# Kernel tuning notes

Hardware: AMD Instinct MI355X
Metric: run time of the kernel (lower is better)

The kernel has to match this reference:

```python
import jax, jax.numpy as jnp
import numpy as np

B, S, D = 2, 1024, 768
H, HD = 12, 64
E, K, F = 8, 2, 3072
EPS = 1e-5


def _ln(x, g, b):
    mu = jnp.mean(x, -1, keepdims=True)
    var = jnp.mean(jnp.square(x - mu), -1, keepdims=True)
    return (x - mu) * jax.lax.rsqrt(var + EPS) * g + b


def setup_inputs() -> dict:
    key = jax.random.key(0)
    ks = jax.random.split(key, 12)
    s = lambda k, shape, sc: jax.random.normal(k, shape, jnp.float32) * sc
    return {
        "hidden_states": s(ks[0], (B, S, D), 1.0),
        "ln1_g": jnp.ones((D,), jnp.float32), "ln1_b": jnp.zeros((D,), jnp.float32),
        "w_attn": s(ks[1], (D, 3 * D), 0.02), "b_attn": jnp.zeros((3 * D,), jnp.float32),
        "w_attnproj": s(ks[2], (D, D), 0.02), "b_attnproj": jnp.zeros((D,), jnp.float32),
        "ln2_g": jnp.ones((D,), jnp.float32), "ln2_b": jnp.zeros((D,), jnp.float32),
        "w_router": s(ks[3], (E, D), 0.01),
        "w_fc": s(ks[4], (E, D, F), 0.02 / E), "b_fc": jnp.zeros((E, F), jnp.float32),
        "w_proj": s(ks[5], (E, F, D), 0.02 / E), "b_proj": jnp.zeros((E, D), jnp.float32),
    }


def reference(hidden_states, ln1_g, ln1_b, w_attn, b_attn, w_attnproj, b_attnproj,
              ln2_g, ln2_b, w_router, w_fc, b_fc, w_proj, b_proj):
    # --- attention sub-block (GPT-2 style, causal) ---
    residual = hidden_states
    x = _ln(hidden_states, ln1_g, ln1_b)
    qkv = x @ w_attn + b_attn                         # [B,S,3D]
    q, k, v = jnp.split(qkv, 3, axis=-1)
    def heads(t):
        return t.reshape(B, S, H, HD).transpose(0, 2, 1, 3)  # [B,H,S,HD]
    q, k, v = heads(q), heads(k), heads(v)
    scores = jnp.einsum("bhqd,bhkd->bhqk", q, k) / np.sqrt(HD).astype(np.float32)
    causal = jnp.tril(jnp.ones((S, S), bool))
    scores = jnp.where(causal, scores, jnp.finfo(scores.dtype).min)
    attn = jax.nn.softmax(scores, axis=-1)
    ctx = jnp.einsum("bhqk,bhkd->bhqd", attn, v)
    ctx = ctx.transpose(0, 2, 1, 3).reshape(B, S, D)
    attn_out = ctx @ w_attnproj + b_attnproj
    hs = attn_out + residual

    # --- MoE FFN sub-block ---
    residual = hs
    x2 = _ln(hs, ln2_g, ln2_b)
    logits = x2 @ w_router.T                          # [B,S,E]
    probs = jax.nn.softmax(logits, axis=-1)
    top_w, top_idx = jax.lax.top_k(probs, K)          # [B,S,K]
    top_w = top_w / jnp.sum(top_w, -1, keepdims=True)
    gates = jnp.sum(jax.nn.one_hot(top_idx, E, dtype=x2.dtype) * top_w[..., None], axis=2)  # [B,S,E]
    h = jax.nn.gelu(jnp.einsum("bsd,edf->bsef", x2, w_fc) + b_fc, approximate=False)
    y = jnp.einsum("bsef,efd->bsed", h, w_proj) + b_proj
    moe_out = jnp.einsum("bse,bsed->bsd", gates, y)
    return moe_out + residual
```

## Files before the change

kernel.cpp:

```cpp
#include <hip/hip_runtime.h>
#include <hip/hip_bf16.h>
#include <math.h>

#define NB 2
#define SEQ 1024
#define DM 768
#define NHEAD 12
#define HDIM 64
#define NEXP 8
#define FF 3072
#define NTOK (NB*SEQ)
#define TDIM (3*DM)
#define LNEPS 1e-5f
#define NSLOT (NTOK*2)

typedef __attribute__((ext_vector_type(8))) short v8s;
typedef __attribute__((ext_vector_type(4))) float v4f;

#define GLDS16(src, dst) \
    __builtin_amdgcn_global_load_lds((const __attribute__((address_space(1))) unsigned int*)(src), \
                                     (__attribute__((address_space(3))) unsigned int*)(dst), 16, 0, 0)

static __device__ __forceinline__ float bf2f(unsigned short u){
    return __uint_as_float(((unsigned)u) << 16);
}
static __device__ __forceinline__ unsigned short f2bf(float f){
    unsigned u = __float_as_uint(f);
    u += 0x7fffu + ((u >> 16) & 1u);
    return (unsigned short)(u >> 16);
}
static __device__ __forceinline__ float gelu_exact(float x){
    return 0.5f * x * (1.0f + erff(x * 0.70710678118654752440f));
}

__global__ __launch_bounds__(256) void tconv_kernel(const float* __restrict__ in,
                                                    unsigned short* __restrict__ out,
                                                    int R, int C){
    __shared__ float T[32][33];
    size_t base = (size_t)blockIdx.z * R * C;
    int c0 = blockIdx.x * 32, r0 = blockIdx.y * 32;
    int t = threadIdx.x;
    int tr = t >> 3, tc4 = (t & 7) * 4;
    float4 v = *(const float4*)&in[base + (size_t)(r0 + tr) * C + c0 + tc4];
    T[tr][tc4+0] = v.x; T[tr][tc4+1] = v.y; T[tr][tc4+2] = v.z; T[tr][tc4+3] = v.w;
    __syncthreads();
    int oc = t >> 3, or4 = (t & 7) * 4;
    ushort4 o;
    o.x = f2bf(T[or4+0][oc]); o.y = f2bf(T[or4+1][oc]);
    o.z = f2bf(T[or4+2][oc]); o.w = f2bf(T[or4+3][oc]);
    *(ushort4*)&out[base + (size_t)(c0 + oc) * R + r0 + or4] = o;
}

__global__ __launch_bounds__(256) void ln_b(const float* __restrict__ in,
                                            const float* __restrict__ g,
// ... 80 lines not shown
    }
    __syncthreads();
    if (tid == 0){
        float lg[NEXP];
        #pragma unroll
        for (int e = 0; e < NEXP; e++)
            lg[e] = wsum[0][e] + wsum[1][e] + wsum[2][e] + wsum[3][e];
        int i0 = 0; float m0 = lg[0];
        #pragma unroll
        for (int e = 1; e < NEXP; e++) if (lg[e] > m0){ m0 = lg[e]; i0 = e; }
        int i1 = -1; float m1 = -INFINITY;
        #pragma unroll
        for (int e = 0; e < NEXP; e++) if (e != i0 && lg[e] > m1){ m1 = lg[e]; i1 = e; }
        float mx = fmaxf(m0, m1);
        float e0 = __expf(m0 - mx), e1 = __expf(m1 - mx);
        float inv = 1.0f / (e0 + e1);
        int p0 = atomicAdd(&cnt[i0], 1);
        int p1 = atomicAdd(&cnt[i1], 1);
        expTok[i0*NTOK + p0] = t;
        expTok[i1*NTOK + p1] = t;
        tokE[t*2]   = i0; tokE[t*2+1]   = i1;
        tokPos[t*2] = p0; tokPos[t*2+1] = p1;
        tokGate[t*2]   = e0 * inv;
        tokGate[t*2+1] = e1 * inv;
    }
}

__global__ __launch_bounds__(256) void mm_qkv(const unsigned short* __restrict__ Ab,
                                              const unsigned short* __restrict__ Bb,
                                              const float* __restrict__ bias,
                                              unsigned short* __restrict__ Qb,
                                              unsigned short* __restrict__ Kb,
                                              unsigned short* __restrict__ Vt){
    __shared__ __align__(16) unsigned short As[64*32];
    __shared__ __align__(16) unsigned short Bs[128*32];
    int bm = blockIdx.y * 64, bn = blockIdx.x * 128;
    int tid = threadIdx.x, wave = tid >> 6, lane = tid & 63;
    int quad = lane >> 4, l15 = lane & 15;
    int wm = wave >> 1, wn = wave & 1;
    int arow = tid >> 2, achunk = (tid & 3) * 8;
    int lrow = lane >> 2, lchunk = (lane & 3) * 8;
    const unsigned short* aS  = Ab + (size_t)(bm + arow) * DM + achunk;
    const unsigned short* bS0 = Bb + (size_t)(bn +      wave*16 + lrow) * DM + lchunk;
    const unsigned short* bS1 = Bb + (size_t)(bn + 64 + wave*16 + lrow) * DM + lchunk;
    unsigned short* aD  = &As[(wave*16)*32];
    unsigned short* bD0 = &Bs[(     wave*16)*32];
    unsigned short* bD1 = &Bs[(64 + wave*16)*32];
    v4f acc[2][4];
    #pragma unroll
    for (int i = 0; i < 2; i++)
        #pragma unroll
        for (int j = 0; j < 4; j++) acc[i][j] = (v4f){0.f,0.f,0.f,0.f};
    for (int kt = 0; kt < DM/32; kt++){
        int kb = kt * 32;
        GLDS16(aS + kb, aD); GLDS16(bS0 + kb, bD0); GLDS16(bS1 + kb, bD1);
        __syncthreads();
        v8s a[2], bfr[4];
        #pragma unroll
        for (int i = 0; i < 2; i++) a[i] = *(const v8s*)&As[(wm*32 + i*16 + l15)*32 + quad*8];
        #pragma unroll
        for (int i = 0; i < 4; i++) bfr[i] = *(const v8s*)&Bs[(wn*64 + i*16 + l15)*32 + quad*8];
        #pragma unroll
        for (int mi = 0; mi < 2; mi++)
            #pragma unroll
            for (int ni = 0; ni < 4; ni++)
                acc[mi][ni] = __builtin_amdgcn_mfma_f32_16x16x32_bf16(a[mi], bfr[ni], acc[mi][ni], 0, 0, 0);
        __syncthreads();
    }
    int btyp = bn / DM;
    #pragma unroll
    for (int ni = 0; ni < 4; ni++){
        int n = bn + wn*64 + ni*16 + l15;
        float bb = bias[n];
        int hd = n % DM; int h = hd >> 6; int d = hd & 63;
        #pragma unroll
        for (int mi = 0; mi < 2; mi++){
            int m = bm + wm*32 + mi*16 + quad*4;
            int b = m >> 10, sd = m & 1023;
            size_t bhbase = (size_t)(b*NHEAD + h);
            if (btyp == 0){
                #pragma unroll
                for (int r = 0; r < 4; r++)
                    Qb[(bhbase*SEQ + sd + r)*HDIM + d] = f2bf((acc[mi][ni][r] + bb) * 0.125f);
            } else if (btyp == 1){
                #pragma unroll
                for (int r = 0; r < 4; r++)
                    Kb[(bhbase*SEQ + sd + r)*HDIM + d] = f2bf(acc[mi][ni][r] + bb);
            } else {
                ushort4 o;
                o.x = f2bf(acc[mi][ni][0] + bb); o.y = f2bf(acc[mi][ni][1] + bb);
                o.z = f2bf(acc[mi][ni][2] + bb); o.w = f2bf(acc[mi][ni][3] + bb);
                *(ushort4*)&Vt[(bhbase*HDIM + d)*SEQ + sd] = o;
            }
        }
    }
}

__global__ __launch_bounds__(64) void fattn(const unsigned short* __restrict__ Qb,
                                            const unsigned short* __restrict__ Kb,
                                            const unsigned short* __restrict__ Vt,
                                            unsigned short* __restrict__ ctxb){
    int bh = blockIdx.x >> 5;
    int q0 = (31 - (blockIdx.x & 31)) * 32;
    int h = bh % NHEAD, b = bh / NHEAD;
    int lane = threadIdx.x;
    int quad = lane >> 4, l15 = lane & 15;

    __shared__ __align__(16) unsigned short Plds[32*32];

    const unsigned short* qp = Qb + ((size_t)bh*SEQ + q0 + l15) * HDIM + quad*8;
    v8s qa00 = *(const v8s*)qp;
    v8s qa01 = *(const v8s*)(qp + 32);
    v8s qa10 = *(const v8s*)(qp + 16*HDIM);
    v8s qa11 = *(const v8s*)(qp + 16*HDIM + 32);

    v4f o[2][4];
    #pragma unroll
    for (int i = 0; i < 2; i++)
        #pragma unroll
        for (int j = 0; j < 4; j++) o[i][j] = (v4f){0.f,0.f,0.f,0.f};
    float mrow[2][4], lrow[2][4];
    #pragma unroll
    for (int i = 0; i < 2; i++)
        #pragma unroll
        for (int r = 0; r < 4; r++){ mrow[i][r] = -1e30f; lrow[i][r] = 0.f; }

    int nch = (q0 >> 5) + 1;
    for (int ch = 0; ch < nch; ch++){
        int kt = ch * 32;
        const unsigned short* kp = Kb + ((size_t)bh*SEQ + kt + l15) * HDIM + quad*8;
        v8s k00 = *(const v8s*)kp;
        v8s k01 = *(const v8s*)(kp + 32);
        v8s k10 = *(const v8s*)(kp + 16*HDIM);
        v8s k11 = *(const v8s*)(kp + 16*HDIM + 32);
        v4f s00 = {0,0,0,0}, s01 = {0,0,0,0}, s10 = {0,0,0,0}, s11 = {0,0,0,0};
        s00 = __builtin_amdgcn_mfma_f32_16x16x32_bf16(qa00, k00, s00, 0, 0, 0);
        s00 = __builtin_amdgcn_mfma_f32_16x16x32_bf16(qa01, k01, s00, 0, 0, 0);
        s01 = __builtin_amdgcn_mfma_f32_16x16x32_bf16(qa00, k10, s01, 0, 0, 0);
        s01 = __builtin_amdgcn_mfma_f32_16x16x32_bf16(qa01, k11, s01, 0, 0, 0);
        s10 = __builtin_amdgcn_mfma_f32_16x16x32_bf16(qa10, k00, s10, 0, 0, 0);
        s10 = __builtin_amdgcn_mfma_f32_16x16x32_bf16(qa11, k01, s10, 0, 0, 0);
        s11 = __builtin_amdgcn_mfma_f32_16x16x32_bf16(qa10, k10, s11, 0, 0, 0);
        s11 = __builtin_amdgcn_mfma_f32_16x16x32_bf16(qa11, k11, s11, 0, 0, 0);

        int key0 = kt + l15, key1 = kt + 16 + l15;
        float alpha[2][4];
        #pragma unroll
        for (int mi = 0; mi < 2; mi++){
            #pragma unroll
            for (int r = 0; r < 4; r++){
                int qrow = q0 + mi*16 + quad*4 + r;
                float sv0 = mi ? s10[r] : s00[r];
                float sv1 = mi ? s11[r] : s01[r];
                float v0 = (key0 <= qrow) ? sv0 : -1e30f;
                float v1 = (key1 <= qrow) ? sv1 : -1e30f;
                float mx = fmaxf(v0, v1);
                mx = fmaxf(mx, __shfl_xor(mx, 1));
                mx = fmaxf(mx, __shfl_xor(mx, 2));
                mx = fmaxf(mx, __shfl_xor(mx, 4));
                mx = fmaxf(mx, __shfl_xor(mx, 8));
                float mn = fmaxf(mrow[mi][r], mx);
                alpha[mi][r] = __expf(mrow[mi][r] - mn);
                float p0 = __expf(v0 - mn);
                float p1 = __expf(v1 - mn);
                float ps = p0 + p1;
                ps += __shfl_xor(ps, 1);
                ps += __shfl_xor(ps, 2);
                ps += __shfl_xor(ps, 4);
                ps += __shfl_xor(ps, 8);
                lrow[mi][r] = lrow[mi][r] * alpha[mi][r] + ps;
                mrow[mi][r] = mn;
                Plds[(mi*16 + quad*4 + r)*32 + l15]      = f2bf(p0);
                Plds[(mi*16 + quad*4 + r)*32 + 16 + l15] = f2bf(p1);
            }
        }
        #pragma unroll
        for (int mi = 0; mi < 2; mi++)
            #pragma unroll
            for (int df = 0; df < 4; df++)
                #pragma unroll
                for (int r = 0; r < 4; r++)
                    o[mi][df][r] *= alpha[mi][r];
        __syncthreads();
        v8s pa0 = *(const v8s*)&Plds[l15*32 + quad*8];
        v8s pa1 = *(const v8s*)&Plds[(16 + l15)*32 + quad*8];
        const unsigned short* vp = Vt + ((size_t)bh*HDIM + l15) * SEQ + kt + quad*8;
        #pragma unroll
        for (int df = 0; df < 4; df++){
            v8s vb = *(const v8s*)(vp + df*16*SEQ);
            o[0][df] = __builtin_amdgcn_mfma_f32_16x16x32_bf16(pa0, vb, o[0][df], 0, 0, 0);
            o[1][df] = __builtin_amdgcn_mfma_f32_16x16x32_bf16(pa1, vb, o[1][df], 0, 0, 0);
        }
        __syncthreads();
    }
    #pragma unroll
    for (int mi = 0; mi < 2; mi++){
        #pragma unroll
        for (int r = 0; r < 4; r++){
            float inv = 1.0f / lrow[mi][r];
            size_t orow = (size_t)(b*SEQ + q0 + mi*16 + quad*4 + r) * DM + h*HDIM;
            #pragma unroll
            for (int df = 0; df < 4; df++)
                ctxb[orow + df*16 + l15] = f2bf(o[mi][df][r] * inv);
        }
    }
}

__global__ __launch_bounds__(256) void mm_attnproj(const unsigned short* __restrict__ Ab,
                                                   const unsigned short* __restrict__ Bb,
                                                   const float* __restrict__ bias,
                                                   const float* __restrict__ res,
                                                   float* __restrict__ C){
    __shared__ __align__(16) unsigned short As[64*32];
    __shared__ __align__(16) unsigned short Bs[64*32];
    int bm = blockIdx.y * 64, bn = blockIdx.x * 64;
    int tid = threadIdx.x, wave = tid >> 6, lane = tid & 63;
    int quad = lane >> 4, l15 = lane & 15;
    int wm = wave >> 1, wn = wave & 1;
    int arow = tid >> 2, achunk = (tid & 3) * 8;
    const unsigned short* aS = Ab + (size_t)(bm + arow) * DM + achunk;
    const unsigned short* bS = Bb + (size_t)(bn + arow) * DM + achunk;
    unsigned short* aD = &As[(wave*16)*32];
    unsigned short* bD = &Bs[(wave*16)*32];
    v4f acc[2][2];
    #pragma unroll
    for (int i = 0; i < 2; i++)
        #pragma unroll
        for (int j = 0; j < 2; j++) acc[i][j] = (v4f){0.f,0.f,0.f,0.f};
    for (int kt = 0; kt < DM/32; kt++){
        int kb = kt * 32;
        GLDS16(aS + kb, aD); GLDS16(bS + kb, bD);
        __syncthreads();
        v8s a[2], bfr[2];
        #pragma unroll
        for (int i = 0; i < 2; i++){
            a[i]   = *(const v8s*)&As[(wm*32 + i*16 + l15)*32 + quad*8];
            bfr[i] = *(const v8s*)&Bs[(wn*32 + i*16 + l15)*32 + quad*8];
        }
        #pragma unroll
        for (int mi = 0; mi < 2; mi++)
            #pragma unroll
            for (int ni = 0; ni < 2; ni++)
                acc[mi][ni] = __builtin_amdgcn_mfma_f32_16x16x32_bf16(a[mi], bfr[ni], acc[mi][ni], 0, 0, 0);
        __syncthreads();
    }
    #pragma unroll
    for (int ni = 0; ni < 2; ni++){
        int n = bn + wn*32 + ni*16 + l15;
        float bb = bias[n];
        #pragma unroll
        for (int mi = 0; mi < 2; mi++){
            int m = bm + wm*32 + mi*16 + quad*4;
            #pragma unroll
            for (int r = 0; r < 4; r++)
                C[(size_t)(m + r) * DM + n] = acc[mi][ni][r] + bb + res[(size_t)(m + r) * DM + n];
        }
    }
}

__global__ __launch_bounds__(256) void mm_fc(const unsigned short* __restrict__ Xb,
                                             const unsigned short* __restrict__ Wb,
                                             const float* __restrict__ bfc,
                                             const int* __restrict__ expTok,
                                             const int* __restrict__ cnt,
                                             const int* __restrict__ offE,
                                             unsigned short* __restrict__ H){
    int e = blockIdx.z, tile = blockIdx.y;
    int c = cnt[e];
    int rows = c - tile * 128;
    if (rows <= 0) return;
    __shared__ __align__(16) unsigned short As[128*32];
    __shared__ __align__(16) unsigned short Bs[128*32];
    __shared__ int toks[128];
    int bn = blockIdx.x * 128;
    int tid = threadIdx.x, wave = tid >> 6, lane = tid & 63;
    if (tid < 128){
        int idx = tile * 128 + tid;
        if (idx >= c) idx = c - 1;
        toks[tid] = expTok[e * NTOK + idx];
    }
    __syncthreads();
    int quad = lane >> 4, l15 = lane & 15;
    int wm = wave >> 1, wn = wave & 1;
    int lrow = lane >> 2, lchunk = (lane & 3) * 8;
    int tok0 = toks[     wave*16 + lrow];
    int tok1 = toks[64 + wave*16 + lrow];
    const unsigned short* Be = Wb + (size_t)e * FF * DM;
    const unsigned short* aS0 = Xb + (size_t)tok0 * DM + lchunk;
    const unsigned short* aS1 = Xb + (size_t)tok1 * DM + lchunk;
    const unsigned short* bS0 = Be + (size_t)(bn +      wave*16 + lrow) * DM + lchunk;
    const unsigned short* bS1 = Be + (size_t)(bn + 64 + wave*16 + lrow) * DM + lchunk;
    unsigned short* aD0 = &As[(     wave*16)*32];
    unsigned short* aD1 = &As[(64 + wave*16)*32];
    unsigned short* bD0 = &Bs[(     wave*16)*32];
    unsigned short* bD1 = &Bs[(64 + wave*16)*32];
    v4f acc[4][4];
    #pragma unroll
    for (int i = 0; i < 4; i++)
        #pragma unroll
        for (int j = 0; j < 4; j++) acc[i][j] = (v4f){0.f,0.f,0.f,0.f};
    for (int kt = 0; kt < DM/32; kt++){
        int kb = kt * 32;
        GLDS16(aS0 + kb, aD0); GLDS16(aS1 + kb, aD1);
        GLDS16(bS0 + kb, bD0); GLDS16(bS1 + kb, bD1);
        __syncthreads();
        v8s a[4], bfr[4];
        #pragma unroll
        for (int i = 0; i < 4; i++){
            a[i]   = *(const v8s*)&As[(wm*64 + i*16 + l15)*32 + quad*8];
            bfr[i] = *(const v8s*)&Bs[(wn*64 + i*16 + l15)*32 + quad*8];
        }
        #pragma unroll
        for (int mt = 0; mt < 4; mt++)
            #pragma unroll
            for (int nt = 0; nt < 4; nt++)
                acc[mt][nt] = __builtin_amdgcn_mfma_f32_16x16x32_bf16(a[mt], bfr[nt], acc[mt][nt], 0, 0, 0);
        __syncthreads();
    }
    int slot0 = offE[e] + tile * 128;
    #pragma unroll
    for (int nt = 0; nt < 4; nt++){
        int n = bn + wn*64 + nt*16 + l15;
        float bb = bfc[(size_t)e * FF + n];
        #pragma unroll
        for (int mt = 0; mt < 4; mt++){
            int ml = wm*64 + mt*16 + quad*4;
            #pragma unroll
            for (int r = 0; r < 4; r++)
                if (ml + r < rows)
                    H[(size_t)(slot0 + ml + r) * FF + n] = f2bf(gelu_exact(acc[mt][nt][r] + bb));
        }
    }
}

__global__ __launch_bounds__(256) void mm_proj(const unsigned short* __restrict__ H,
                                               const unsigned short* __restrict__ Wb,
                                               const int* __restrict__ cnt,
                                               const int* __restrict__ offE,
                                               float* __restrict__ Yp){
    int e = blockIdx.z, tile = blockIdx.y;
    int c = cnt[e];
    int rows = c - tile * 64;
    if (rows <= 0) return;
    int sk = blockIdx.x & 1;
    int bn = (blockIdx.x >> 1) * 128;
    __shared__ __align__(16) unsigned short As[64*32];
    __shared__ __align__(16) unsigned short Bs[128*32];
    int tid = threadIdx.x, wave = tid >> 6, lane = tid & 63;
    int quad = lane >> 4, l15 = lane & 15;
    int wm = wave >> 1, wn = wave & 1;
    int slot0 = offE[e] + tile * 64;
    int arow = tid >> 2, achunk = (tid & 3) * 8;
    int arl = arow < rows ? arow : rows - 1;
    int lrow = lane >> 2, lchunk = (lane & 3) * 8;
    const unsigned short* Be = Wb + (size_t)e * DM * FF;
    const unsigned short* aS  = H  + (size_t)(slot0 + arl) * FF + sk*1536 + achunk;
    const unsigned short* bS0 = Be + (size_t)(bn +      wave*16 + lrow) * FF + sk*1536 + lchunk;
    const unsigned short* bS1 = Be + (size_t)(bn + 64 + wave*16 + lrow) * FF + sk*1536 + lchunk;
    unsigned short* aD  = &As[(wave*16)*32];
    unsigned short* bD0 = &Bs[(     wave*16)*32];
    unsigned short* bD1 = &Bs[(64 + wave*16)*32];
    v4f acc[2][4];
    #pragma unroll
    for (int i = 0; i < 2; i++)
        #pragma unroll
        for (int j = 0; j < 4; j++) acc[i][j] = (v4f){0.f,0.f,0.f,0.f};
    for (int kt = 0; kt < 1536/32; kt++){
        int kb = kt * 32;
        GLDS16(aS + kb, aD); GLDS16(bS0 + kb, bD0); GLDS16(bS1 + kb, bD1);
        __syncthreads();
        v8s a[2], bfr[4];
        #pragma unroll
        for (int i = 0; i < 2; i++) a[i] = *(const v8s*)&As[(wm*32 + i*16 + l15)*32 + quad*8];
        #pragma unroll
        for (int i = 0; i < 4; i++) bfr[i] = *(const v8s*)&Bs[(wn*64 + i*16 + l15)*32 + quad*8];
        #pragma unroll
        for (int mi = 0; mi < 2; mi++)
            #pragma unroll
            for (int ni = 0; ni < 4; ni++)
                acc[mi][ni] = __builtin_amdgcn_mfma_f32_16x16x32_bf16(a[mi], bfr[ni], acc[mi][ni], 0, 0, 0);
        __syncthreads();
    }
    float* Yo = Yp + (size_t)sk * NSLOT * DM;
    #pragma unroll
    for (int ni = 0; ni < 4; ni++){
        int n = bn + wn*64 + ni*16 + l15;
        #pragma unroll
        for (int mi = 0; mi < 2; mi++){
            int ml = wm*32 + mi*16 + quad*4;
            #pragma unroll
            for (int r = 0; r < 4; r++)
                if (ml + r < rows)
                    Yo[(size_t)(slot0 + ml + r) * DM + n] = acc[mi][ni][r];
        }
    }
}

__global__ void offsets_kernel(const int* __restrict__ cnt, int* __restrict__ offE){
    if (threadIdx.x == 0 && blockIdx.x == 0){
        int a = 0;
        for (int e = 0; e < NEXP; e++){ offE[e] = a; a += cnt[e]; }
    }
}

__global__ __launch_bounds__(256) void combine_kernel(const float* __restrict__ hs,
                                                      const float* __restrict__ Yp,
                                                      const float* __restrict__ bproj,
                                                      const int* __restrict__ tokE,
                                                      const int* __restrict__ tokPos,
                                                      const float* __restrict__ tokGate,
                                                      const int* __restrict__ offE,
                                                      float* __restrict__ out){
    int t = blockIdx.x;
    int e0 = tokE[t*2], e1 = tokE[t*2+1];
// ... 33 lines not shown
    const float* b_proj  = (const float*)d_in[13];
    float* out = (float*)d_out;

    char* ws = (char*)d_ws;
    float*          hs   = (float*)(ws + 0);
    unsigned short* xb   = (unsigned short*)(ws + 6291456);
    unsigned short* Qb   = (unsigned short*)(ws + 9437184);
    unsigned short* Kb   = (unsigned short*)(ws + 12582912);
    unsigned short* Vt   = (unsigned short*)(ws + 15728640);
    unsigned short* ctxb = (unsigned short*)(ws + 18874368);
    unsigned short* Wab  = (unsigned short*)(ws + 22020096);
    unsigned short* Wapb = (unsigned short*)(ws + 25559040);
    unsigned short* H    = (unsigned short*)(ws + 9437184);
    unsigned short* Wfcb = (unsigned short*)(ws + 34603008);
    unsigned short* Wprb = (unsigned short*)(ws + 72351744);
    float*          Yp   = (float*)(ws + 34603008);
    char* rt = ws + 110100480;
    int* cnt      = (int*)(rt + 0);
    int* offE     = (int*)(rt + 64);
    int* expTok   = (int*)(rt + 128);
    int* tokE     = (int*)(rt + 128 + 65536);
    int* tokPos   = (int*)(rt + 128 + 81920);
    float* tokGate= (float*)(rt + 128 + 98304);

    hipMemsetAsync(cnt, 0, NEXP * sizeof(int), stream);

    tconv_kernel<<<dim3(TDIM/32, DM/32, 1), 256, 0, stream>>>(w_attn, Wab, DM, TDIM);
    tconv_kernel<<<dim3(DM/32, DM/32, 1), 256, 0, stream>>>(w_aproj, Wapb, DM, DM);
    tconv_kernel<<<dim3(FF/32, DM/32, NEXP), 256, 0, stream>>>(w_fc, Wfcb, DM, FF);
    tconv_kernel<<<dim3(DM/32, FF/32, NEXP), 256, 0, stream>>>(w_proj, Wprb, FF, DM);

    ln_b<<<NTOK, 256, 0, stream>>>(hidden, ln1_g, ln1_b, xb);
    mm_qkv<<<dim3(TDIM/128, NTOK/64), 256, 0, stream>>>(xb, Wab, b_attn, Qb, Kb, Vt);
    fattn<<<NB*NHEAD*32, 64, 0, stream>>>(Qb, Kb, Vt, ctxb);
    mm_attnproj<<<dim3(DM/64, NTOK/64), 256, 0, stream>>>(ctxb, Wapb, b_aproj, hidden, hs);
    ln_router<<<NTOK, 256, 0, stream>>>(hs, ln2_g, ln2_b, w_rout, xb,
                                        cnt, expTok, tokE, tokPos, tokGate);
    offsets_kernel<<<1, 64, 0, stream>>>(cnt, offE);
    mm_fc<<<dim3(FF/128, NTOK/128, NEXP), 256, 0, stream>>>(xb, Wfcb, b_fc, expTok, cnt, offE, H);
    mm_proj<<<dim3((DM/128)*2, NTOK/64, NEXP), 256, 0, stream>>>(H, Wprb, cnt, offE, Yp);
    combine_kernel<<<NTOK, 256, 0, stream>>>(hs, Yp, b_proj, tokE, tokPos, tokGate, offE, out);
}
```

Baseline: 483.6 us.

## Double-buffer LDS tiles with async global-to-LDS prefetch in all GEMM kernels

Converts the QKV, attention-projection, expert FC and expert projection GEMM loops from single-buffered LDS staging to a two-stage ping-pong scheme. The next K-slice is issued with global_load_lds while the current one is being consumed by MFMAs, using explicit vmcnt waits and raw barriers. The goal is to hide global memory latency behind matrix math. In exchange, LDS use per block doubles, which may lower occupancy, and the hand-written waitcnt counts must match the number of outstanding loads for the results to stay correct.

```diff
diff --git a/kernel.cpp b/kernel.cpp
--- a/kernel.cpp
+++ b/kernel.cpp
@@ -20,6 +20,9 @@
 #define GLDS16(src, dst) \
     __builtin_amdgcn_global_load_lds((const __attribute__((address_space(1))) unsigned int*)(src), \
                                      (__attribute__((address_space(3))) unsigned int*)(dst), 16, 0, 0)
+
+#define BARF() do { asm volatile("" ::: "memory"); __builtin_amdgcn_s_barrier(); asm volatile("" ::: "memory"); } while(0)
+#define WAITV(n) asm volatile("s_waitcnt vmcnt(" #n ")" ::: "memory")
 
 static __device__ __forceinline__ float bf2f(unsigned short u){
     return __uint_as_float(((unsigned)u) << 16);
@@ -166,8 +169,8 @@
                                               unsigned short* __restrict__ Qb,
                                               unsigned short* __restrict__ Kb,
                                               unsigned short* __restrict__ Vt){
-    __shared__ __align__(16) unsigned short As[64*32];
-    __shared__ __align__(16) unsigned short Bs[128*32];
+    __shared__ __align__(16) unsigned short As[2][64*32];
+    __shared__ __align__(16) unsigned short Bs[2][128*32];
     int bm = blockIdx.y * 64, bn = blockIdx.x * 128;
     int tid = threadIdx.x, wave = tid >> 6, lane = tid & 63;
     int quad = lane >> 4, l15 = lane & 15;
@@ -177,29 +180,44 @@
     const unsigned short* aS  = Ab + (size_t)(bm + arow) * DM + achunk;
     const unsigned short* bS0 = Bb + (size_t)(bn +      wave*16 + lrow) * DM + lchunk;
     const unsigned short* bS1 = Bb + (size_t)(bn + 64 + wave*16 + lrow) * DM + lchunk;
-    unsigned short* aD  = &As[(wave*16)*32];
-    unsigned short* bD0 = &Bs[(     wave*16)*32];
-    unsigned short* bD1 = &Bs[(64 + wave*16)*32];
     v4f acc[2][4];
     #pragma unroll
     for (int i = 0; i < 2; i++)
         #pragma unroll
         for (int j = 0; j < 4; j++) acc[i][j] = (v4f){0.f,0.f,0.f,0.f};
-    for (int kt = 0; kt < DM/32; kt++){
-        int kb = kt * 32;
-        GLDS16(aS + kb, aD); GLDS16(bS0 + kb, bD0); GLDS16(bS1 + kb, bD1);
-        __syncthreads();
-        v8s a[2], bfr[4];
-        #pragma unroll
-        for (int i = 0; i < 2; i++) a[i] = *(const v8s*)&As[(wm*32 + i*16 + l15)*32 + quad*8];
-        #pragma unroll
-        for (int i = 0; i < 4; i++) bfr[i] = *(const v8s*)&Bs[(wn*64 + i*16 + l15)*32 + quad*8];
-        #pragma unroll
-        for (int mi = 0; mi < 2; mi++)
-            #pragma unroll
-            for (int ni = 0; ni < 4; ni++)
-                acc[mi][ni] = __builtin_amdgcn_mfma_f32_16x16x32_bf16(a[mi], bfr[ni], acc[mi][ni], 0, 0, 0);
-        __syncthreads();
+
+#define QKV_STAGE(buf, kb) do { \
+    GLDS16(aS  + (kb), &As[buf][(wave*16)*32]); \
+    GLDS16(bS0 + (kb), &Bs[buf][(     wave*16)*32]); \
+    GLDS16(bS1 + (kb), &Bs[buf][(64 + wave*16)*32]); \
+} while(0)
+#define QKV_COMP(buf) do { \
+    v8s a[2], bfr[4]; \
+    _Pragma("unroll") \
+    for (int i = 0; i < 2; i++) a[i] = *(const v8s*)&As[buf][(wm*32 + i*16 + l15)*32 + quad*8]; \
+    _Pragma("unroll") \
+    for (int i = 0; i < 4; i++) bfr[i] = *(const v8s*)&Bs[buf][(wn*64 + i*16 + l15)*32 + quad*8]; \
+    _Pragma("unroll") \
+    for (int mi = 0; mi < 2; mi++) \
+        _Pragma("unroll") \
+        for (int ni = 0; ni < 4; ni++) \
+            acc[mi][ni] = __builtin_amdgcn_mfma_f32_16x16x32_bf16(a[mi], bfr[ni], acc[mi][ni], 0, 0, 0); \
+} while(0)
+
+    const int NK = DM/32;
+    QKV_STAGE(0, 0);
+    #pragma unroll 1
+    for (int kt = 0; kt < NK; kt += 2){
+        QKV_STAGE(1, (kt+1)*32);
+        WAITV(3);
+        BARF();
+        QKV_COMP(0);
+        BARF();
+        if (kt + 2 < NK){ QKV_STAGE(0, (kt+2)*32); WAITV(3); }
+        else            { WAITV(0); }
+        BARF();
+        QKV_COMP(1);
+        BARF();
     }
     int btyp = bn / DM;
     #pragma unroll
@@ -345,8 +363,8 @@
                                                    const float* __restrict__ bias,
                                                    const float* __restrict__ res,
                                                    float* __restrict__ C){
-    __shared__ __align__(16) unsigned short As[64*32];
-    __shared__ __align__(16) unsigned short Bs[64*32];
+    __shared__ __align__(16) unsigned short As[2][64*32];
+    __shared__ __align__(16) unsigned short Bs[2][64*32];
     int bm = blockIdx.y * 64, bn = blockIdx.x * 64;
     int tid = threadIdx.x, wave = tid >> 6, lane = tid & 63;
     int quad = lane >> 4, l15 = lane & 15;
@@ -354,29 +372,44 @@
     int arow = tid >> 2, achunk = (tid & 3) * 8;
     const unsigned short* aS = Ab + (size_t)(bm + arow) * DM + achunk;
     const unsigned short* bS = Bb + (size_t)(bn + arow) * DM + achunk;
-    unsigned short* aD = &As[(wave*16)*32];
-    unsigned short* bD = &Bs[(wave*16)*32];
     v4f acc[2][2];
     #pragma unroll
     for (int i = 0; i < 2; i++)
         #pragma unroll
         for (int j = 0; j < 2; j++) acc[i][j] = (v4f){0.f,0.f,0.f,0.f};
-    for (int kt = 0; kt < DM/32; kt++){
-        int kb = kt * 32;
-        GLDS16(aS + kb, aD); GLDS16(bS + kb, bD);
-        __syncthreads();
-        v8s a[2], bfr[2];
-        #pragma unroll
-        for (int i = 0; i < 2; i++){
-            a[i]   = *(const v8s*)&As[(wm*32 + i*16 + l15)*32 + quad*8];
-            bfr[i] = *(const v8s*)&Bs[(wn*32 + i*16 + l15)*32 + quad*8];
-        }
-        #pragma unroll
-        for (int mi = 0; mi < 2; mi++)
-            #pragma unroll
-            for (int ni = 0; ni < 2; ni++)
-                acc[mi][ni] = __builtin_amdgcn_mfma_f32_16x16x32_bf16(a[mi], bfr[ni], acc[mi][ni], 0, 0, 0);
-        __syncthreads();
+
+#define AP_STAGE(buf, kb) do { \
+    GLDS16(aS + (kb), &As[buf][(wave*16)*32]); \
+    GLDS16(bS + (kb), &Bs[buf][(wave*16)*32]); \
+} while(0)
+#define AP_COMP(buf) do { \
+    v8s a[2], bfr[2]; \
+    _Pragma("unroll") \
+    for (int i = 0; i < 2; i++){ \
+        a[i]   = *(const v8s*)&As[buf][(wm*32 + i*16 + l15)*32 + quad*8]; \
+        bfr[i] = *(const v8s*)&Bs[buf][(wn*32 + i*16 + l15)*32 + quad*8]; \
+    } \
+    _Pragma("unroll") \
+    for (int mi = 0; mi < 2; mi++) \
+        _Pragma("unroll") \
+        for (int ni = 0; ni < 2; ni++) \
+            acc[mi][ni] = __builtin_amdgcn_mfma_f32_16x16x32_bf16(a[mi], bfr[ni], acc[mi][ni], 0, 0, 0); \
+} while(0)
+
+    const int NK = DM/32;
+    AP_STAGE(0, 0);
+    #pragma unroll 1
+    for (int kt = 0; kt < NK; kt += 2){
+        AP_STAGE(1, (kt+1)*32);
+        WAITV(2);
+        BARF();
+        AP_COMP(0);
+        BARF();
+        if (kt + 2 < NK){ AP_STAGE(0, (kt+2)*32); WAITV(2); }
+        else            { WAITV(0); }
+        BARF();
+        AP_COMP(1);
+        BARF();
     }
     #pragma unroll
     for (int ni = 0; ni < 2; ni++){
@@ -403,8 +436,8 @@
     int c = cnt[e];
     int rows = c - tile * 128;
     if (rows <= 0) return;
-    __shared__ __align__(16) unsigned short As[128*32];
-    __shared__ __align__(16) unsigned short Bs[128*32];
+    __shared__ __align__(16) unsigned short As[2][128*32];
+    __shared__ __align__(16) unsigned short Bs[2][128*32];
     __shared__ int toks[128];
     int bn = blockIdx.x * 128;
     int tid = threadIdx.x, wave = tid >> 6, lane = tid & 63;
@@ -424,32 +457,46 @@
     const unsigned short* aS1 = Xb + (size_t)tok1 * DM + lchunk;
     const unsigned short* bS0 = Be + (size_t)(bn +      wave*16 + lrow) * DM + lchunk;
     const unsigned short* bS1 = Be + (size_t)(bn + 64 + wave*16 + lrow) * DM + lchunk;
-    unsigned short* aD0 = &As[(     wave*16)*32];
-    unsigned short* aD1 = &As[(64 + wave*16)*32];
-    unsigned short* bD0 = &Bs[(     wave*16)*32];
-    unsigned short* bD1 = &Bs[(64 + wave*16)*32];
     v4f acc[4][4];
     #pragma unroll
     for (int i = 0; i < 4; i++)
         #pragma unroll
         for (int j = 0; j < 4; j++) acc[i][j] = (v4f){0.f,0.f,0.f,0.f};
-    for (int kt = 0; kt < DM/32; kt++){
-        int kb = kt * 32;
-        GLDS16(aS0 + kb, aD0); GLDS16(aS1 + kb, aD1);
-        GLDS16(bS0 + kb, bD0); GLDS16(bS1 + kb, bD1);
-        __syncthreads();
-        v8s a[4], bfr[4];
-        #pragma unroll
-        for (int i = 0; i < 4; i++){
-            a[i]   = *(const v8s*)&As[(wm*64 + i*16 + l15)*32 + quad*8];
-            bfr[i] = *(const v8s*)&Bs[(wn*64 + i*16 + l15)*32 + quad*8];
-        }
-        #pragma unroll
-        for (int mt = 0; mt < 4; mt++)
-            #pragma unroll
-            for (int nt = 0; nt < 4; nt++)
-                acc[mt][nt] = __builtin_amdgcn_mfma_f32_16x16x32_bf16(a[mt], bfr[nt], acc[mt][nt], 0, 0, 0);
-        __syncthreads();
+
+#define FC_STAGE(buf, kb) do { \
+    GLDS16(aS0 + (kb), &As[buf][(     wave*16)*32]); \
+    GLDS16(aS1 + (kb), &As[buf][(64 + wave*16)*32]); \
+    GLDS16(bS0 + (kb), &Bs[buf][(     wave*16)*32]); \
+    GLDS16(bS1 + (kb), &Bs[buf][(64 + wave*16)*32]); \
+} while(0)
+#define FC_COMP(buf) do { \
+    v8s a[4], bfr[4]; \
+    _Pragma("unroll") \
+    for (int i = 0; i < 4; i++){ \
+        a[i]   = *(const v8s*)&As[buf][(wm*64 + i*16 + l15)*32 + quad*8]; \
+        bfr[i] = *(const v8s*)&Bs[buf][(wn*64 + i*16 + l15)*32 + quad*8]; \
+    } \
+    _Pragma("unroll") \
+    for (int mt = 0; mt < 4; mt++) \
+        _Pragma("unroll") \
+        for (int nt = 0; nt < 4; nt++) \
+            acc[mt][nt] = __builtin_amdgcn_mfma_f32_16x16x32_bf16(a[mt], bfr[nt], acc[mt][nt], 0, 0, 0); \
+} while(0)
+
+    const int NK = DM/32;
+    FC_STAGE(0, 0);
+    #pragma unroll 1
+    for (int kt = 0; kt < NK; kt += 2){
+        FC_STAGE(1, (kt+1)*32);
+        WAITV(4);
+        BARF();
+        FC_COMP(0);
+        BARF();
+        if (kt + 2 < NK){ FC_STAGE(0, (kt+2)*32); WAITV(4); }
+        else            { WAITV(0); }
+        BARF();
+        FC_COMP(1);
+        BARF();
     }
     int slot0 = offE[e] + tile * 128;
     #pragma unroll
@@ -478,8 +525,8 @@
     if (rows <= 0) return;
     int sk = blockIdx.x & 1;
     int bn = (blockIdx.x >> 1) * 128;
-    __shared__ __align__(16) unsigned short As[64*32];
-    __shared__ __align__(16) unsigned short Bs[128*32];
+    __shared__ __align__(16) unsigned short As[2][64*32];
+    __shared__ __align__(16) unsigned short Bs[2][128*32];
     int tid = threadIdx.x, wave = tid >> 6, lane = tid & 63;
     int quad = lane >> 4, l15 = lane & 15;
     int wm = wave >> 1, wn = wave & 1;
@@ -491,29 +538,44 @@
     const unsigned short* aS  = H  + (size_t)(slot0 + arl) * FF + sk*1536 + achunk;
     const unsigned short* bS0 = Be + (size_t)(bn +      wave*16 + lrow) * FF + sk*1536 + lchunk;
     const unsigned short* bS1 = Be + (size_t)(bn + 64 + wave*16 + lrow) * FF + sk*1536 + lchunk;
-    unsigned short* aD  = &As[(wave*16)*32];
-    unsigned short* bD0 = &Bs[(     wave*16)*32];
-    unsigned short* bD1 = &Bs[(64 + wave*16)*32];
     v4f acc[2][4];
     #pragma unroll
     for (int i = 0; i < 2; i++)
         #pragma unroll
         for (int j = 0; j < 4; j++) acc[i][j] = (v4f){0.f,0.f,0.f,0.f};
-    for (int kt = 0; kt < 1536/32; kt++){
-        int kb = kt * 32;
-        GLDS16(aS + kb, aD); GLDS16(bS0 + kb, bD0); GLDS16(bS1 + kb, bD1);
-        __syncthreads();
-        v8s a[2], bfr[4];
-        #pragma unroll
-        for (int i = 0; i < 2; i++) a[i] = *(const v8s*)&As[(wm*32 + i*16 + l15)*32 + quad*8];
-        #pragma unroll
-        for (int i = 0; i < 4; i++) bfr[i] = *(const v8s*)&Bs[(wn*64 + i*16 + l15)*32 + quad*8];
-        #pragma unroll
-        for (int mi = 0; mi < 2; mi++)
-            #pragma unroll
-            for (int ni = 0; ni < 4; ni++)
-                acc[mi][ni] = __builtin_amdgcn_mfma_f32_16x16x32_bf16(a[mi], bfr[ni], acc[mi][ni], 0, 0, 0);
-        __syncthreads();
+
+#define PJ_STAGE(buf, kb) do { \
+    GLDS16(aS  + (kb), &As[buf][(wave*16)*32]); \
+    GLDS16(bS0 + (kb), &Bs[buf][(     wave*16)*32]); \
+    GLDS16(bS1 + (kb), &Bs[buf][(64 + wave*16)*32]); \
+} while(0)
+#define PJ_COMP(buf) do { \
+    v8s a[2], bfr[4]; \
+    _Pragma("unroll") \
+    for (int i = 0; i < 2; i++) a[i] = *(const v8s*)&As[buf][(wm*32 + i*16 + l15)*32 + quad*8]; \
+    _Pragma("unroll") \
+    for (int i = 0; i < 4; i++) bfr[i] = *(const v8s*)&Bs[buf][(wn*64 + i*16 + l15)*32 + quad*8]; \
+    _Pragma("unroll") \
+    for (int mi = 0; mi < 2; mi++) \
+        _Pragma("unroll") \
+        for (int ni = 0; ni < 4; ni++) \
+            acc[mi][ni] = __builtin_amdgcn_mfma_f32_16x16x32_bf16(a[mi], bfr[ni], acc[mi][ni], 0, 0, 0); \
+} while(0)
+
+    const int NK = 1536/32;
+    PJ_STAGE(0, 0);
+    #pragma unroll 1
+    for (int kt = 0; kt < NK; kt += 2){
+        PJ_STAGE(1, (kt+1)*32);
+        WAITV(3);
+        BARF();
+        PJ_COMP(0);
+        BARF();
+        if (kt + 2 < NK){ PJ_STAGE(0, (kt+2)*32); WAITV(3); }
+        else            { WAITV(0); }
+        BARF();
+        PJ_COMP(1);
+        BARF();
     }
     float* Yo = Yp + (size_t)sk * NSLOT * DM;
     #pragma unroll
```

Result: no change. 485.3 us (+0.4%).

## Load GEMM fragments directly from global memory and shrink attention and FC tiles

Applied to the files above, without the earlier changes.

All four GEMM kernels drop their LDS staging (global_load_lds plus two barriers per k-step). Each wave now loads its MFMA operand fragments straight from global memory, with the k-loop unrolled by two, which removes the synchronization overhead. Flash attention moves from 32 to 16 query rows per block, doubling the grid for better load balance. The MoE FC tile shrinks from 128 to 64 rows to cut padding waste on uneven expert counts. The cost is that operands are no longer shared through LDS, so waves re-read the same A/B rows from global or L2, and the smaller tiles raise total memory traffic.

```diff
diff --git a/kernel.cpp b/kernel.cpp
--- a/kernel.cpp
+++ b/kernel.cpp
@@ -17,9 +17,7 @@
 typedef __attribute__((ext_vector_type(8))) short v8s;
 typedef __attribute__((ext_vector_type(4))) float v4f;
 
-#define GLDS16(src, dst) \
-    __builtin_amdgcn_global_load_lds((const __attribute__((address_space(1))) unsigned int*)(src), \
-                                     (__attribute__((address_space(3))) unsigned int*)(dst), 16, 0, 0)
+#define MFMA(a,b,c) __builtin_amdgcn_mfma_f32_16x16x32_bf16((a),(b),(c),0,0,0)
 
 static __device__ __forceinline__ float bf2f(unsigned short u){
     return __uint_as_float(((unsigned)u) << 16);
@@ -166,40 +164,36 @@
                                               unsigned short* __restrict__ Qb,
                                               unsigned short* __restrict__ Kb,
                                               unsigned short* __restrict__ Vt){
-    __shared__ __align__(16) unsigned short As[64*32];
-    __shared__ __align__(16) unsigned short Bs[128*32];
     int bm = blockIdx.y * 64, bn = blockIdx.x * 128;
     int tid = threadIdx.x, wave = tid >> 6, lane = tid & 63;
     int quad = lane >> 4, l15 = lane & 15;
     int wm = wave >> 1, wn = wave & 1;
-    int arow = tid >> 2, achunk = (tid & 3) * 8;
-    int lrow = lane >> 2, lchunk = (lane & 3) * 8;
-    const unsigned short* aS  = Ab + (size_t)(bm + arow) * DM + achunk;
-    const unsigned short* bS0 = Bb + (size_t)(bn +      wave*16 + lrow) * DM + lchunk;
-    const unsigned short* bS1 = Bb + (size_t)(bn + 64 + wave*16 + lrow) * DM + lchunk;
-    unsigned short* aD  = &As[(wave*16)*32];
-    unsigned short* bD0 = &Bs[(     wave*16)*32];
-    unsigned short* bD1 = &Bs[(64 + wave*16)*32];
+    const unsigned short* aP[2];
+    const unsigned short* bP[4];
+    #pragma unroll
+    for (int mi = 0; mi < 2; mi++)
+        aP[mi] = Ab + (size_t)(bm + wm*32 + mi*16 + l15) * DM + quad*8;
+    #pragma unroll
+    for (int ni = 0; ni < 4; ni++)
+        bP[ni] = Bb + (size_t)(bn + wn*64 + ni*16 + l15) * DM + quad*8;
     v4f acc[2][4];
     #pragma unroll
     for (int i = 0; i < 2; i++)
         #pragma unroll
         for (int j = 0; j < 4; j++) acc[i][j] = (v4f){0.f,0.f,0.f,0.f};
+    #pragma unroll 2
     for (int kt = 0; kt < DM/32; kt++){
         int kb = kt * 32;
-        GLDS16(aS + kb, aD); GLDS16(bS0 + kb, bD0); GLDS16(bS1 + kb, bD1);
-        __syncthreads();
-        v8s a[2], bfr[4];
-        #pragma unroll
-        for (int i = 0; i < 2; i++) a[i] = *(const v8s*)&As[(wm*32 + i*16 + l15)*32 + quad*8];
-        #pragma unroll
-        for (int i = 0; i < 4; i++) bfr[i] = *(const v8s*)&Bs[(wn*64 + i*16 + l15)*32 + quad*8];
+        v8s a[2], bf[4];
+        #pragma unroll
+        for (int mi = 0; mi < 2; mi++) a[mi] = *(const v8s*)(aP[mi] + kb);
+        #pragma unroll
+        for (int ni = 0; ni < 4; ni++) bf[ni] = *(const v8s*)(bP[ni] + kb);
         #pragma unroll
         for (int mi = 0; mi < 2; mi++)
             #pragma unroll
             for (int ni = 0; ni < 4; ni++)
-                acc[mi][ni] = __builtin_amdgcn_mfma_f32_16x16x32_bf16(a[mi], bfr[ni], acc[mi][ni], 0, 0, 0);
-        __syncthreads();
+                acc[mi][ni] = MFMA(a[mi], bf[ni], acc[mi][ni]);
     }
     int btyp = bn / DM;
     #pragma unroll
@@ -234,30 +228,24 @@
                                             const unsigned short* __restrict__ Kb,
                                             const unsigned short* __restrict__ Vt,
                                             unsigned short* __restrict__ ctxb){
-    int bh = blockIdx.x >> 5;
-    int q0 = (31 - (blockIdx.x & 31)) * 32;
+    int bh = blockIdx.x >> 6;
+    int q0 = (63 - (blockIdx.x & 63)) * 16;
     int h = bh % NHEAD, b = bh / NHEAD;
     int lane = threadIdx.x;
     int quad = lane >> 4, l15 = lane & 15;
 
-    __shared__ __align__(16) unsigned short Plds[32*32];
+    __shared__ __align__(16) unsigned short Plds[16*32];
 
     const unsigned short* qp = Qb + ((size_t)bh*SEQ + q0 + l15) * HDIM + quad*8;
-    v8s qa00 = *(const v8s*)qp;
-    v8s qa01 = *(const v8s*)(qp + 32);
-    v8s qa10 = *(const v8s*)(qp + 16*HDIM);
-    v8s qa11 = *(const v8s*)(qp + 16*HDIM + 32);
-
-    v4f o[2][4];
-    #pragma unroll
-    for (int i = 0; i < 2; i++)
-        #pragma unroll
-        for (int j = 0; j < 4; j++) o[i][j] = (v4f){0.f,0.f,0.f,0.f};
-    float mrow[2][4], lrow[2][4];
-    #pragma unroll
-    for (int i = 0; i < 2; i++)
-        #pragma unroll
-        for (int r = 0; r < 4; r++){ mrow[i][r] = -1e30f; lrow[i][r] = 0.f; }
+    v8s qa0 = *(const v8s*)qp;
+    v8s qa1 = *(const v8s*)(qp + 32);
+
+    v4f o[4];
+    #pragma unroll
+    for (int j = 0; j < 4; j++) o[j] = (v4f){0.f,0.f,0.f,0.f};
+    float mrow[4], lrow[4];
+    #pragma unroll
+    for (int r = 0; r < 4; r++){ mrow[r] = -1e30f; lrow[r] = 0.f; }
 
     int nch = (q0 >> 5) + 1;
     for (int ch = 0; ch < nch; ch++){
@@ -267,76 +255,58 @@
         v8s k01 = *(const v8s*)(kp + 32);
         v8s k10 = *(const v8s*)(kp + 16*HDIM);
         v8s k11 = *(const v8s*)(kp + 16*HDIM + 32);
-        v4f s00 = {0,0,0,0}, s01 = {0,0,0,0}, s10 = {0,0,0,0}, s11 = {0,0,0,0};
-        s00 = __builtin_amdgcn_mfma_f32_16x16x32_bf16(qa00, k00, s00, 0, 0, 0);
-        s00 = __builtin_amdgcn_mfma_f32_16x16x32_bf16(qa01, k01, s00, 0, 0, 0);
-        s01 = __builtin_amdgcn_mfma_f32_16x16x32_bf16(qa00, k10, s01, 0, 0, 0);
-        s01 = __builtin_amdgcn_mfma_f32_16x16x32_bf16(qa01, k11, s01, 0, 0, 0);
-        s10 = __builtin_amdgcn_mfma_f32_16x16x32_bf16(qa10, k00, s10, 0, 0, 0);
-        s10 = __builtin_amdgcn_mfma_f32_16x16x32_bf16(qa11, k01, s10, 0, 0, 0);
-        s11 = __builtin_amdgcn_mfma_f32_16x16x32_bf16(qa10, k10, s11, 0, 0, 0);
-        s11 = __builtin_amdgcn_mfma_f32_16x16x32_bf16(qa11, k11, s11, 0, 0, 0);
+        v4f s0 = {0,0,0,0}, s1 = {0,0,0,0};
+        s0 = MFMA(qa0, k00, s0); s0 = MFMA(qa1, k01, s0);
+        s1 = MFMA(qa0, k10, s1); s1 = MFMA(qa1, k11, s1);
 
         int key0 = kt + l15, key1 = kt + 16 + l15;
-        float alpha[2][4];
-        #pragma unroll
-        for (int mi = 0; mi < 2; mi++){
-            #pragma unroll
-            for (int r = 0; r < 4; r++){
-                int qrow = q0 + mi*16 + quad*4 + r;
-                float sv0 = mi ? s10[r] : s00[r];
-                float sv1 = mi ? s11[r] : s01[r];
-                float v0 = (key0 <= qrow) ? sv0 : -1e30f;
-                float v1 = (key1 <= qrow) ? sv1 : -1e30f;
-                float mx = fmaxf(v0, v1);
-                mx = fmaxf(mx, __shfl_xor(mx, 1));
-                mx = fmaxf(mx, __shfl_xor(mx, 2));
-                mx = fmaxf(mx, __shfl_xor(mx, 4));
-                mx = fmaxf(mx, __shfl_xor(mx, 8));
-                float mn = fmaxf(mrow[mi][r], mx);
-                alpha[mi][r] = __expf(mrow[mi][r] - mn);
-                float p0 = __expf(v0 - mn);
-                float p1 = __expf(v1 - mn);
-                float ps = p0 + p1;
-                ps += __shfl_xor(ps, 1);
-                ps += __shfl_xor(ps, 2);
-                ps += __shfl_xor(ps, 4);
-                ps += __shfl_xor(ps, 8);
-                lrow[mi][r] = lrow[mi][r] * alpha[mi][r] + ps;
-                mrow[mi][r] = mn;
-                Plds[(mi*16 + quad*4 + r)*32 + l15]      = f2bf(p0);
-                Plds[(mi*16 + quad*4 + r)*32 + 16 + l15] = f2bf(p1);
-            }
+        float alpha[4];
+        #pragma unroll
+        for (int r = 0; r < 4; r++){
+            int qrow = q0 + quad*4 + r;
+            float v0 = (key0 <= qrow) ? s0[r] : -1e30f;
+            float v1 = (key1 <= qrow) ? s1[r] : -1e30f;
+            float mx = fmaxf(v0, v1);
+            mx = fmaxf(mx, __shfl_xor(mx, 1));
+            mx = fmaxf(mx, __shfl_xor(mx, 2));
+            mx = fmaxf(mx, __shfl_xor(mx, 4));
+            mx = fmaxf(mx, __shfl_xor(mx, 8));
+            float mn = fmaxf(mrow[r], mx);
+            alpha[r] = __expf(mrow[r] - mn);
+            float p0 = __expf(v0 - mn);
+            float p1 = __expf(v1 - mn);
+            float ps = p0 + p1;
+            ps += __shfl_xor(ps, 1);
+            ps += __shfl_xor(ps, 2);
+            ps += __shfl_xor(ps, 4);
+            ps += __shfl_xor(ps, 8);
+            lrow[r] = lrow[r] * alpha[r] + ps;
+            mrow[r] = mn;
+            Plds[(quad*4 + r)*32 + l15]      = f2bf(p0);
+            Plds[(quad*4 + r)*32 + 16 + l15] = f2bf(p1);
         }
         #pragma unroll
-        for (int mi = 0; mi < 2; mi++)
-            #pragma unroll
-            for (int df = 0; df < 4; df++)
-                #pragma unroll
-                for (int r = 0; r < 4; r++)
-                    o[mi][df][r] *= alpha[mi][r];
+        for (int df = 0; df < 4; df++)
+            #pragma unroll
+            for (int r = 0; r < 4; r++)
+                o[df][r] *= alpha[r];
         __syncthreads();
         v8s pa0 = *(const v8s*)&Plds[l15*32 + quad*8];
-        v8s pa1 = *(const v8s*)&Plds[(16 + l15)*32 + quad*8];
         const unsigned short* vp = Vt + ((size_t)bh*HDIM + l15) * SEQ + kt + quad*8;
         #pragma unroll
         for (int df = 0; df < 4; df++){
             v8s vb = *(const v8s*)(vp + df*16*SEQ);
-            o[0][df] = __builtin_amdgcn_mfma_f32_16x16x32_bf16(pa0, vb, o[0][df], 0, 0, 0);
-            o[1][df] = __builtin_amdgcn_mfma_f32_16x16x32_bf16(pa1, vb, o[1][df], 0, 0, 0);
+            o[df] = MFMA(pa0, vb, o[df]);
         }
         __syncthreads();
     }
     #pragma unroll
-    for (int mi = 0; mi < 2; mi++){
-        #pragma unroll
-        for (int r = 0; r < 4; r++){
-            float inv = 1.0f / lrow[mi][r];
-            size_t orow = (size_t)(b*SEQ + q0 + mi*16 + quad*4 + r) * DM + h*HDIM;
-            #pragma unroll
-            for (int df = 0; df < 4; df++)
-                ctxb[orow + df*16 + l15] = f2bf(o[mi][df][r] * inv);
-        }
+    for (int r = 0; r < 4; r++){
+        float inv = 1.0f / lrow[r];
+        size_t orow = (size_t)(b*SEQ + q0 + quad*4 + r) * DM + h*HDIM;
+        #pragma unroll
+        for (int df = 0; df < 4; df++)
+            ctxb[orow + df*16 + l15] = f2bf(o[df][r] * inv);
     }
 }
 
@@ -345,38 +315,36 @@
                                                    const float* __restrict__ bias,
                                                    const float* __restrict__ res,
                                                    float* __restrict__ C){
-    __shared__ __align__(16) unsigned short As[64*32];
-    __shared__ __align__(16) unsigned short Bs[64*32];
     int bm = blockIdx.y * 64, bn = blockIdx.x * 64;
     int tid = threadIdx.x, wave = tid >> 6, lane = tid & 63;
     int quad = lane >> 4, l15 = lane & 15;
     int wm = wave >> 1, wn = wave & 1;
-    int arow = tid >> 2, achunk = (tid & 3) * 8;
-    const unsigned short* aS = Ab + (size_t)(bm + arow) * DM + achunk;
-    const unsigned short* bS = Bb + (size_t)(bn + arow) * DM + achunk;
-    unsigned short* aD = &As[(wave*16)*32];
-    unsigned short* bD = &Bs[(wave*16)*32];
+    const unsigned short* aP[2];
+    const unsigned short* bP[2];
+    #pragma unroll
+    for (int mi = 0; mi < 2; mi++)
+        aP[mi] = Ab + (size_t)(bm + wm*32 + mi*16 + l15) * DM + quad*8;
+    #pragma unroll
+    for (int ni = 0; ni < 2; ni++)
+        bP[ni] = Bb + (size_t)(bn + wn*32 + ni*16 + l15) * DM + quad*8;
     v4f acc[2][2];
     #pragma unroll
     for (int i = 0; i < 2; i++)
         #pragma unroll
         for (int j = 0; j < 2; j++) acc[i][j] = (v4f){0.f,0.f,0.f,0.f};
+    #pragma unroll 2
     for (int kt = 0; kt < DM/32; kt++){
         int kb = kt * 32;
-        GLDS16(aS + kb, aD); GLDS16(bS + kb, bD);
-        __syncthreads();
-        v8s a[2], bfr[2];
-        #pragma unroll
-        for (int i = 0; i < 2; i++){
-            a[i]   = *(const v8s*)&As[(wm*32 + i*16 + l15)*32 + quad*8];
-            bfr[i] = *(const v8s*)&Bs[(wn*32 + i*16 + l15)*32 + quad*8];
-        }
+        v8s a[2], bf[2];
+        #pragma unroll
+        for (int mi = 0; mi < 2; mi++) a[mi] = *(const v8s*)(aP[mi] + kb);
+        #pragma unroll
+        for (int ni = 0; ni < 2; ni++) bf[ni] = *(const v8s*)(bP[ni] + kb);
         #pragma unroll
         for (int mi = 0; mi < 2; mi++)
             #pragma unroll
             for (int ni = 0; ni < 2; ni++)
-                acc[mi][ni] = __builtin_amdgcn_mfma_f32_16x16x32_bf16(a[mi], bfr[ni], acc[mi][ni], 0, 0, 0);
-        __syncthreads();
+                acc[mi][ni] = MFMA(a[mi], bf[ni], acc[mi][ni]);
     }
     #pragma unroll
     for (int ni = 0; ni < 2; ni++){
@@ -401,68 +369,56 @@
                                              unsigned short* __restrict__ H){
     int e = blockIdx.z, tile = blockIdx.y;
     int c = cnt[e];
-    int rows = c - tile * 128;
+    int rows = c - tile * 64;
     if (rows <= 0) return;
-    __shared__ __align__(16) unsigned short As[128*32];
-    __shared__ __align__(16) unsigned short Bs[128*32];
-    __shared__ int toks[128];
     int bn = blockIdx.x * 128;
     int tid = threadIdx.x, wave = tid >> 6, lane = tid & 63;
-    if (tid < 128){
-        int idx = tile * 128 + tid;
-        if (idx >= c) idx = c - 1;
-        toks[tid] = expTok[e * NTOK + idx];
-    }
-    __syncthreads();
     int quad = lane >> 4, l15 = lane & 15;
     int wm = wave >> 1, wn = wave & 1;
-    int lrow = lane >> 2, lchunk = (lane & 3) * 8;
-    int tok0 = toks[     wave*16 + lrow];
-    int tok1 = toks[64 + wave*16 + lrow];
     const unsigned short* Be = Wb + (size_t)e * FF * DM;
-    const unsigned short* aS0 = Xb + (size_t)tok0 * DM + lchunk;
-    const unsigned short* aS1 = Xb + (size_t)tok1 * DM + lchunk;
-    const unsigned short* bS0 = Be + (size_t)(bn +      wave*16 + lrow) * DM + lchunk;
-    const unsigned short* bS1 = Be + (size_t)(bn + 64 + wave*16 + lrow) * DM + lchunk;
-    unsigned short* aD0 = &As[(     wave*16)*32];
-    unsigned short* aD1 = &As[(64 + wave*16)*32];
-    unsigned short* bD0 = &Bs[(     wave*16)*32];
-    unsigned short* bD1 = &Bs[(64 + wave*16)*32];
-    v4f acc[4][4];
-    #pragma unroll
-    for (int i = 0; i < 4; i++)
+    const unsigned short* aP[2];
+    const unsigned short* bP[4];
+    #pragma unroll
+    for (int mi = 0; mi < 2; mi++){
+        int rr = tile*64 + wm*32 + mi*16 + l15;
+        if (rr >= c) rr = c - 1;
+        int tok = expTok[e*NTOK + rr];
+        aP[mi] = Xb + (size_t)tok * DM + quad*8;
+    }
+    #pragma unroll
+    for (int ni = 0; ni < 4; ni++)
+        bP[ni] = Be + (size_t)(bn + wn*64 + ni*16 + l15) * DM + quad*8;
+    v4f acc[2][4];
+    #pragma unroll
+    for (int i = 0; i < 2; i++)
         #pragma unroll
         for (int j = 0; j < 4; j++) acc[i][j] = (v4f){0.f,0.f,0.f,0.f};
+    #pragma unroll 2
     for (int kt = 0; kt < DM/32; kt++){
         int kb = kt * 32;
-        GLDS16(aS0 + kb, aD0); GLDS16(aS1 + kb, aD1);
-        GLDS16(bS0 + kb, bD0); GLDS16(bS1 + kb, bD1);
-        __syncthreads();
-        v8s a[4], bfr[4];
-        #pragma unroll
-        for (int i = 0; i < 4; i++){
-            a[i]   = *(const v8s*)&As[(wm*64 + i*16 + l15)*32 + quad*8];
-            bfr[i] = *(const v8s*)&Bs[(wn*64 + i*16 + l15)*32 + quad*8];
-        }
-        #pragma unroll
-        for (int mt = 0; mt < 4; mt++)
-            #pragma unroll
-            for (int nt = 0; nt < 4; nt++)
-                acc[mt][nt] = __builtin_amdgcn_mfma_f32_16x16x32_bf16(a[mt], bfr[nt], acc[mt][nt], 0, 0, 0);
-        __syncthreads();
-    }
-    int slot0 = offE[e] + tile * 128;
-    #pragma unroll
-    for (int nt = 0; nt < 4; nt++){
-        int n = bn + wn*64 + nt*16 + l15;
+        v8s a[2], bf[4];
+        #pragma unroll
+        for (int mi = 0; mi < 2; mi++) a[mi] = *(const v8s*)(aP[mi] + kb);
+        #pragma unroll
+        for (int ni = 0; ni < 4; ni++) bf[ni] = *(const v8s*)(bP[ni] + kb);
+        #pragma unroll
+        for (int mi = 0; mi < 2; mi++)
+            #pragma unroll
+            for (int ni = 0; ni < 4; ni++)
+                acc[mi][ni] = MFMA(a[mi], bf[ni], acc[mi][ni]);
+    }
+    int slot0 = offE[e] + tile * 64;
+    #pragma unroll
+    for (int ni = 0; ni < 4; ni++){
+        int n = bn + wn*64 + ni*16 + l15;
         float bb = bfc[(size_t)e * FF + n];
         #pragma unroll
-        for (int mt = 0; mt < 4; mt++){
-            int ml = wm*64 + mt*16 + quad*4;
+        for (int mi = 0; mi < 2; mi++){
+            int ml = wm*32 + mi*16 + quad*4;
             #pragma unroll
             for (int r = 0; r < 4; r++)
                 if (ml + r < rows)
-                    H[(size_t)(slot0 + ml + r) * FF + n] = f2bf(gelu_exact(acc[mt][nt][r] + bb));
+                    H[(size_t)(slot0 + ml + r) * FF + n] = f2bf(gelu_exact(acc[mi][ni][r] + bb));
         }
     }
 }
@@ -478,42 +434,40 @@
     if (rows <= 0) return;
     int sk = blockIdx.x & 1;
     int bn = (blockIdx.x >> 1) * 128;
-    __shared__ __align__(16) unsigned short As[64*32];
-    __shared__ __align__(16) unsigned short Bs[128*32];
     int tid = threadIdx.x, wave = tid >> 6, lane = tid & 63;
     int quad = lane >> 4, l15 = lane & 15;
     int wm = wave >> 1, wn = wave & 1;
     int slot0 = offE[e] + tile * 64;
-    int arow = tid >> 2, achunk = (tid & 3) * 8;
-    int arl = arow < rows ? arow : rows - 1;
-    int lrow = lane >> 2, lchunk = (lane & 3) * 8;
     const unsigned short* Be = Wb + (size_t)e * DM * FF;
-    const unsigned short* aS  = H  + (size_t)(slot0 + arl) * FF + sk*1536 + achunk;
-    const unsigned short* bS0 = Be + (size_t)(bn +      wave*16 + lrow) * FF + sk*1536 + lchunk;
-    const unsigned short* bS1 = Be + (size_t)(bn + 64 + wave*16 + lrow) * FF + sk*1536 + lchunk;
-    unsigned short* aD  = &As[(wave*16)*32];
-    unsigned short* bD0 = &Bs[(     wave*16)*32];
-    unsigned short* bD1 = &Bs[(64 + wave*16)*32];
+    const unsigned short* aP[2];
+    const unsigned short* bP[4];
+    #pragma unroll
+    for (int mi = 0; mi < 2; mi++){
+        int rr = wm*32 + mi*16 + l15;
+        if (rr >= rows) rr = rows - 1;
+        aP[mi] = H + (size_t)(slot0 + rr) * FF + sk*1536 + quad*8;
+    }
+    #pragma unroll
+    for (int ni = 0; ni < 4; ni++)
+        bP[ni] = Be + (size_t)(bn + wn*64 + ni*16 + l15) * FF + sk*1536 + quad*8;
     v4f acc[2][4];
     #pragma unroll
     for (int i = 0; i < 2; i++)
         #pragma unroll
         for (int j = 0; j < 4; j++) acc[i][j] = (v4f){0.f,0.f,0.f,0.f};
+    #pragma unroll 2
     for (int kt = 0; kt < 1536/32; kt++){
         int kb = kt * 32;
-        GLDS16(aS + kb, aD); GLDS16(bS0 + kb, bD0); GLDS16(bS1 + kb, bD1);
-        __syncthreads();
-        v8s a[2], bfr[4];
-        #pragma unroll
-        for (int i = 0; i < 2; i++) a[i] = *(const v8s*)&As[(wm*32 + i*16 + l15)*32 + quad*8];
-        #pragma unroll
-        for (int i = 0; i < 4; i++) bfr[i] = *(const v8s*)&Bs[(wn*64 + i*16 + l15)*32 + quad*8];
+        v8s a[2], bf[4];
+        #pragma unroll
+        for (int mi = 0; mi < 2; mi++) a[mi] = *(const v8s*)(aP[mi] + kb);
+        #pragma unroll
+        for (int ni = 0; ni < 4; ni++) bf[ni] = *(const v8s*)(bP[ni] + kb);
         #pragma unroll
         for (int mi = 0; mi < 2; mi++)
             #pragma unroll
             for (int ni = 0; ni < 4; ni++)
-                acc[mi][ni] = __builtin_amdgcn_mfma_f32_16x16x32_bf16(a[mi], bfr[ni], acc[mi][ni], 0, 0, 0);
-        __syncthreads();
+                acc[mi][ni] = MFMA(a[mi], bf[ni], acc[mi][ni]);
     }
     float* Yo = Yp + (size_t)sk * NSLOT * DM;
     #pragma unroll
@@ -613,12 +567,12 @@
 
     ln_b<<<NTOK, 256, 0, stream>>>(hidden, ln1_g, ln1_b, xb);
     mm_qkv<<<dim3(TDIM/128, NTOK/64), 256, 0, stream>>>(xb, Wab, b_attn, Qb, Kb, Vt);
-    fattn<<<NB*NHEAD*32, 64, 0, stream>>>(Qb, Kb, Vt, ctxb);
+    fattn<<<NB*NHEAD*64, 64, 0, stream>>>(Qb, Kb, Vt, ctxb);
     mm_attnproj<<<dim3(DM/64, NTOK/64), 256, 0, stream>>>(ctxb, Wapb, b_aproj, hidden, hs);
     ln_router<<<NTOK, 256, 0, stream>>>(hs, ln2_g, ln2_b, w_rout, xb,
                                         cnt, expTok, tokE, tokPos, tokGate);
     offsets_kernel<<<1, 64, 0, stream>>>(cnt, offE);
-    mm_fc<<<dim3(FF/128, NTOK/128, NEXP), 256, 0, stream>>>(xb, Wfcb, b_fc, expTok, cnt, offE, H);
+    mm_fc<<<dim3(FF/128, NTOK/64, NEXP), 256, 0, stream>>>(xb, Wfcb, b_fc, expTok, cnt, offE, H);
     mm_proj<<<dim3((DM/128)*2, NTOK/64, NEXP), 256, 0, stream>>>(H, Wprb, cnt, offE, Yp);
     combine_kernel<<<NTOK, 256, 0, stream>>>(hs, Yp, b_proj, tokE, tokPos, tokGate, offE, out);
 }
```

Result: slower. 659.9 us (+36.4%).
